# Optimization experiments

Hardware: AMD Instinct MI355X
Metric: run time of the kernel (lower is better)

The kernel has to match this reference:

```python
import jax, jax.numpy as jnp
import numpy as np

N = 512          # input_dim (nodes, fully connected)
T = 16           # time_dim
F = 4            # feature_dim
D = T * F        # node_attr_dim = 64
B = 16           # batch
NEG_SLOPE = 0.2  # GATv2Conv default


def setup_inputs() -> dict:
    key = jax.random.key(0)
    ks = jax.random.split(key, 10)
    s = 0.05
    return {
        "inputs": jax.random.normal(ks[0], (B, N * D), dtype=jnp.float32),
        "Wl": jax.random.normal(ks[1], (D, D), dtype=jnp.float32) * s,  # lin_l weight
        "bl": jax.random.normal(ks[2], (D,), dtype=jnp.float32) * s,
        "Wr": jax.random.normal(ks[3], (D, D), dtype=jnp.float32) * s,  # lin_r weight
        "br": jax.random.normal(ks[4], (D,), dtype=jnp.float32) * s,
        "att": jax.random.normal(ks[5], (D,), dtype=jnp.float32) * s,   # attention vector a
        "bias": jax.random.normal(ks[6], (D,), dtype=jnp.float32) * s,  # GATv2 output bias
        "Wf": jax.random.normal(ks[7], (1, D), dtype=jnp.float32) * s,  # fusion Linear
        "bf": jax.random.normal(ks[8], (1,), dtype=jnp.float32) * s,
    }


def reference(inputs, Wl, bl, Wr, br, att, bias, Wf, bf):
    # GATv2Conv (heads=1) over a fully-connected graph -> dense attention per sample.
    def per_sample(x_flat):
        x = x_flat.reshape(N, D)              # [N, D] node features
        xl = x @ Wl.T + bl                    # source-side transform (lin_l)
        xr = x @ Wr.T + br                    # target-side transform (lin_r)
        # edge (j -> i): e_ij = a . leaky_relu(xl[j] + xr[i])
        s = jax.nn.leaky_relu(xr[:, None, :] + xl[None, :, :], NEG_SLOPE)  # [i, j, d]
        e = jnp.einsum('ijd,d->ij', s, att)   # [N, N] scores
        alpha = jax.nn.softmax(e, axis=-1)    # softmax over sources j per target i
        out = alpha @ xl + bias               # [N, D] aggregated messages
        fused = out @ Wf.T + bf               # [N, 1] fusion linear
        return fused[:, 0]                    # [N]

    return jax.vmap(per_sample)(inputs)       # [B, N]
```

## Files before the change

kernel.cpp:

```cpp
#include <hip/hip_runtime.h>
#include <hip/hip_fp16.h>

#define BB 16
#define NN 512
#define DD 64
#define ROWS (BB * NN)
#define RB 32
#define JCH 32
#define CHUNK (NN / JCH)

static __device__ __forceinline__ __half2 h2bits(unsigned int u) {
    union { unsigned int i; __half2 h; } c; c.i = u; return c.h;
}
static __device__ __forceinline__ unsigned int bits2(__half2 h) {
    union { __half2 h; unsigned int i; } c; c.h = h; return c.i;
}
static __device__ __forceinline__ __half2 absterm(unsigned int s, unsigned int u,
                                                  unsigned int v, __half2 a) {
    return __hfma2(h2bits(s), __habs2(__hadd2(h2bits(u), h2bits(v))), a);
}

__global__ __launch_bounds__(256, 2) void k1_transform(
    const float* __restrict__ x,
    const float* __restrict__ Wl, const float* __restrict__ bl,
    const float* __restrict__ Wr, const float* __restrict__ br,
    const float* __restrict__ att, const float* __restrict__ bias,
    const float* __restrict__ Wf, const float* __restrict__ bf,
    unsigned int* __restrict__ uh, unsigned int* __restrict__ vh,
    float2* __restrict__ epj,
    unsigned int* __restrict__ sgnh, float* __restrict__ cterm)
{
    __shared__ float wt[64][132];
    __shared__ float xst[64][36];
    __shared__ float red[RB][16][2];

    const int tid = threadIdx.x;
    const int r0 = blockIdx.x * RB;

    #pragma unroll
    for (int t = 0; t < 8; ++t) {
        const int idx = t * 256 + tid;
        const int c   = idx & 127;
        const int k4  = (idx >> 7) << 2;
        const float* src = (c < 64) ? (Wl + c * DD + k4) : (Wr + (c - 64) * DD + k4);
        const float4 v = *reinterpret_cast<const float4*>(src);
        wt[k4 + 0][c] = v.x;
        wt[k4 + 1][c] = v.y;
        wt[k4 + 2][c] = v.z;
        wt[k4 + 3][c] = v.w;
    }
    #pragma unroll
    for (int p = 0; p < 2; ++p) {
        const int idx = p * 256 + tid;
        const int row = idx >> 4;
        const int k4  = (idx & 15) << 2;
        const float4 v = *reinterpret_cast<const float4*>(&x[(size_t)(r0 + row) * DD + k4]);
        xst[k4 + 0][row] = v.x;
        xst[k4 + 1][row] = v.y;
        xst[k4 + 2][row] = v.z;
        xst[k4 + 3][row] = v.w;
    }
    __syncthreads();

    const int g  = tid & 31;
    const int rq = tid >> 5;
    const int c0 = g * 4;
    const int ra = rq * 4;
    const bool isL = (c0 < 64);
    const int d0 = c0 & 63;

    const float4 bv = *reinterpret_cast<const float4*>((isL ? bl : br) + d0);
    float acc[4][4];
    #pragma unroll
    for (int r = 0; r < 4; ++r) {
        acc[r][0] = bv.x; acc[r][1] = bv.y; acc[r][2] = bv.z; acc[r][3] = bv.w;
    }

    #pragma unroll 4
    for (int k = 0; k < 64; ++k) {
        const float4 w4 = *reinterpret_cast<const float4*>(&wt[k][c0]);
        const float4 x4 = *reinterpret_cast<const float4*>(&xst[k][ra]);
        acc[0][0] = fmaf(x4.x, w4.x, acc[0][0]);
        acc[0][1] = fmaf(x4.x, w4.y, acc[0][1]);
        acc[0][2] = fmaf(x4.x, w4.z, acc[0][2]);
        acc[0][3] = fmaf(x4.x, w4.w, acc[0][3]);
        acc[1][0] = fmaf(x4.y, w4.x, acc[1][0]);
        acc[1][1] = fmaf(x4.y, w4.y, acc[1][1]);
        acc[1][2] = fmaf(x4.y, w4.z, acc[1][2]);
        acc[1][3] = fmaf(x4.y, w4.w, acc[1][3]);
        acc[2][0] = fmaf(x4.z, w4.x, acc[2][0]);
        acc[2][1] = fmaf(x4.z, w4.y, acc[2][1]);
        acc[2][2] = fmaf(x4.z, w4.z, acc[2][2]);
        acc[2][3] = fmaf(x4.z, w4.w, acc[2][3]);
        acc[3][0] = fmaf(x4.w, w4.x, acc[3][0]);
        acc[3][1] = fmaf(x4.w, w4.y, acc[3][1]);
        acc[3][2] = fmaf(x4.w, w4.z, acc[3][2]);
        acc[3][3] = fmaf(x4.w, w4.w, acc[3][3]);
    }

    const float4 av = *reinterpret_cast<const float4*>(&att[d0]);

    if (isL) {
        const float4 wfv = *reinterpret_cast<const float4*>(&Wf[d0]);
        #pragma unroll
        for (int r = 0; r < 4; ++r) {
            red[ra + r][g][0] = av.x * acc[r][0] + av.y * acc[r][1] + av.z * acc[r][2] + av.w * acc[r][3];
            red[ra + r][g][1] = wfv.x * acc[r][0] + wfv.y * acc[r][1] + wfv.z * acc[r][2] + wfv.w * acc[r][3];
        }
    }

    unsigned int* const dst = isL ? vh : uh;
    const int q    = d0 >> 3;
    const int slot = (d0 & 4) ? 2 : 0;
    const int base = ((r0 >> 9) * 8 + q) * 512 + (r0 & 511);
    #pragma unroll
    for (int r = 0; r < 4; ++r) {
        uint2 pk;
        pk.x = bits2(__floats2half2_rn(0.4f * av.x * acc[r][0], 0.4f * av.y * acc[r][1]));
        pk.y = bits2(__floats2half2_rn(0.4f * av.z * acc[r][2], 0.4f * av.w * acc[r][3]));
        *reinterpret_cast<uint2*>(&dst[(size_t)(base + ra + r) * 4 + slot]) = pk;
    }
    __syncthreads();

    if (tid < RB) {
        float a = 0.f, p = 0.f;
        #pragma unroll
        for (int gg = 0; gg < 16; ++gg) {
            a += red[tid][gg][0];
            p += red[tid][gg][1];
        }
        const float E = __expf(0.6f * a);
        epj[r0 + tid] = make_float2(E, E * p);
    }

    if (blockIdx.x == 0) {
        if (tid < 32) {
            const float s0 = (att[2 * tid]     >= 0.f) ? 1.f : -1.f;
            const float s1 = (att[2 * tid + 1] >= 0.f) ? 1.f : -1.f;
            sgnh[tid] = bits2(__floats2half2_rn(s0, s1));
        }
        if (tid == 0) {
            float ct = bf[0];
            #pragma unroll 8
            for (int d = 0; d < DD; ++d) ct = fmaf(bias[d], Wf[d], ct);
            *cterm = ct;
        }
    }
}

__global__ __launch_bounds__(512, 2) void k2_attn(
    const unsigned int* __restrict__ uh, const unsigned int* __restrict__ vh,
    const float2* __restrict__ epj, const unsigned int* __restrict__ sgnh,
    float2* __restrict__ part)
{
    const int b  = blockIdx.x >> 5;
    const int jc = blockIdx.x & 31;
    const int i  = threadIdx.x;

    uint4 uu[8];
    #pragma unroll
    for (int q = 0; q < 8; ++q)
        uu[q] = *reinterpret_cast<const uint4*>(&uh[(size_t)(((b * 8 + q) << 9) + i) * 4]);

    uint4 sg[8];
    #pragma unroll
    for (int q = 0; q < 8; ++q)
        sg[q] = reinterpret_cast<const uint4*>(sgnh)[q];

    float s = 0.f, sp = 0.f;
    const int j0 = jc * CHUNK;

    #pragma unroll 2
    for (int jj = 0; jj < CHUNK; ++jj) {
        const int j = j0 + jj;
        __half2 a0 = __float2half2_rn(0.f), a1 = a0;
        #pragma unroll
        for (int q = 0; q < 8; ++q) {
            const uint4 vq = *reinterpret_cast<const uint4*>(
                &vh[(size_t)(((b * 8 + q) << 9) + j) * 4]);
            a0 = absterm(sg[q].x, uu[q].x, vq.x, a0);
            a1 = absterm(sg[q].y, uu[q].y, vq.y, a1);
            a0 = absterm(sg[q].z, uu[q].z, vq.z, a0);
            a1 = absterm(sg[q].w, uu[q].w, vq.w, a1);
        }
        const __half2 h = __hadd2(a0, a1);
        const float f = __low2float(h) + __high2float(h);
        const float t = __expf(f);
        const float2 ep = epj[(b << 9) + j];
        s  = fmaf(t, ep.x, s);
        sp = fmaf(t, ep.y, sp);
    }
    part[(size_t)(((b << 5) + jc) << 9) + i] = make_float2(s, sp);
}

__global__ __launch_bounds__(256) void k3_final(
    const float2* __restrict__ part, const float* __restrict__ cterm,
    float* __restrict__ out)
{
    const int t = blockIdx.x * 256 + threadIdx.x;
    const int b = t >> 9, i = t & 511;
    float s = 0.f, sp = 0.f;
    #pragma unroll
    for (int jc = 0; jc < JCH; ++jc) {
        const float2 v = part[(size_t)(((b << 5) + jc) << 9) + i];
        s  += v.x;
        sp += v.y;
    }
    out[t] = sp / s + *cterm;
}

extern "C" void kernel_launch(void* const* d_in, const int* in_sizes, int n_in,
                              void* d_out, int out_size, void* d_ws, size_t ws_size,
                              hipStream_t stream) {
    const float* x    = (const float*)d_in[0];
    const float* Wl   = (const float*)d_in[1];
    const float* bl   = (const float*)d_in[2];
    const float* Wr   = (const float*)d_in[3];
    const float* br   = (const float*)d_in[4];
    const float* att  = (const float*)d_in[5];
    const float* bias = (const float*)d_in[6];
    const float* Wf   = (const float*)d_in[7];
    const float* bf   = (const float*)d_in[8];
    float* out = (float*)d_out;

    unsigned char* ws = (unsigned char*)d_ws;
    unsigned int* uh   = (unsigned int*)ws;
    unsigned int* vh   = uh + (size_t)ROWS * 32;
    float2*       part = (float2*)(vh + (size_t)ROWS * 32);
    float2*       epj  = part + (size_t)BB * JCH * NN;
    unsigned int* sgnh = (unsigned int*)(epj + ROWS);
    float*        ctp  = (float*)(sgnh + 32);

    k1_transform<<<ROWS / RB, 256, 0, stream>>>(x, Wl, bl, Wr, br, att, bias, Wf, bf,
                                                uh, vh, epj, sgnh, ctp);
    k2_attn<<<BB * JCH, 512, 0, stream>>>(uh, vh, epj, sgnh, part);
    k3_final<<<ROWS / 256, 256, 0, stream>>>(part, ctp, out);
}
```

Baseline: 29.72 us.

## Pre-transpose weights in a prep kernel and halve rows per transform block

Result: slower. 34.63 us (+16.5%).

```diff
diff --git a/kernel.cpp b/kernel.cpp
--- a/kernel.cpp
+++ b/kernel.cpp
@@ -5,7 +5,7 @@
 #define NN 512
 #define DD 64
 #define ROWS (BB * NN)
-#define RB 32
+#define RB 16
 #define JCH 32
 #define CHUNK (NN / JCH)
 
@@ -20,40 +20,56 @@
     return __hfma2(h2bits(s), __habs2(__hadd2(h2bits(u), h2bits(v))), a);
 }
 
-__global__ __launch_bounds__(256, 2) void k1_transform(
-    const float* __restrict__ x,
-    const float* __restrict__ Wl, const float* __restrict__ bl,
-    const float* __restrict__ Wr, const float* __restrict__ br,
+__global__ __launch_bounds__(256) void k0_prep(
+    const float* __restrict__ Wl, const float* __restrict__ Wr,
     const float* __restrict__ att, const float* __restrict__ bias,
     const float* __restrict__ Wf, const float* __restrict__ bf,
+    float* __restrict__ wtg, unsigned int* __restrict__ sgnh,
+    float* __restrict__ cterm)
+{
+    const int idx = blockIdx.x * 256 + threadIdx.x;
+    const int c   = idx >> 4;
+    const int k4  = (idx & 15) << 2;
+    const float* src = (c < 64) ? (Wl + c * DD + k4) : (Wr + (c - 64) * DD + k4);
+    const float4 v = *reinterpret_cast<const float4*>(src);
+    wtg[(k4 + 0) * 128 + c] = v.x;
+    wtg[(k4 + 1) * 128 + c] = v.y;
+    wtg[(k4 + 2) * 128 + c] = v.z;
+    wtg[(k4 + 3) * 128 + c] = v.w;
+
+    if (blockIdx.x == 0) {
+        const int tid = threadIdx.x;
+        if (tid < 32) {
+            const float s0 = (att[2 * tid]     >= 0.f) ? 1.f : -1.f;
+            const float s1 = (att[2 * tid + 1] >= 0.f) ? 1.f : -1.f;
+            sgnh[tid] = bits2(__floats2half2_rn(s0, s1));
+        }
+        if (tid == 0) {
+            float ct = bf[0];
+            #pragma unroll 8
+            for (int d = 0; d < DD; ++d) ct = fmaf(bias[d], Wf[d], ct);
+            *cterm = ct;
+        }
+    }
+}
+
+__global__ __launch_bounds__(256) void k1_transform(
+    const float* __restrict__ x, const float* __restrict__ wtg,
+    const float* __restrict__ bl, const float* __restrict__ br,
+    const float* __restrict__ att, const float* __restrict__ Wf,
     unsigned int* __restrict__ uh, unsigned int* __restrict__ vh,
-    float2* __restrict__ epj,
-    unsigned int* __restrict__ sgnh, float* __restrict__ cterm)
-{
-    __shared__ float wt[64][132];
-    __shared__ float xst[64][36];
-    __shared__ float red[RB][16][2];
+    float2* __restrict__ epj)
+{
+    __shared__ float xst[64][20];
+    __shared__ float red[16][16][2];
 
     const int tid = threadIdx.x;
     const int r0 = blockIdx.x * RB;
-
-    #pragma unroll
-    for (int t = 0; t < 8; ++t) {
-        const int idx = t * 256 + tid;
-        const int c   = idx & 127;
-        const int k4  = (idx >> 7) << 2;
-        const float* src = (c < 64) ? (Wl + c * DD + k4) : (Wr + (c - 64) * DD + k4);
-        const float4 v = *reinterpret_cast<const float4*>(src);
-        wt[k4 + 0][c] = v.x;
-        wt[k4 + 1][c] = v.y;
-        wt[k4 + 2][c] = v.z;
-        wt[k4 + 3][c] = v.w;
-    }
-    #pragma unroll
-    for (int p = 0; p < 2; ++p) {
-        const int idx = p * 256 + tid;
-        const int row = idx >> 4;
-        const int k4  = (idx & 15) << 2;
+    const int b  = blockIdx.x >> 5;
+
+    {
+        const int row = tid >> 4;
+        const int k4  = (tid & 15) << 2;
         const float4 v = *reinterpret_cast<const float4*>(&x[(size_t)(r0 + row) * DD + k4]);
         xst[k4 + 0][row] = v.x;
         xst[k4 + 1][row] = v.y;
@@ -65,37 +81,29 @@
     const int g  = tid & 31;
     const int rq = tid >> 5;
     const int c0 = g * 4;
-    const int ra = rq * 4;
+    const int ra = rq * 2;
     const bool isL = (c0 < 64);
     const int d0 = c0 & 63;
 
     const float4 bv = *reinterpret_cast<const float4*>((isL ? bl : br) + d0);
-    float acc[4][4];
-    #pragma unroll
-    for (int r = 0; r < 4; ++r) {
+    float acc[2][4];
+    #pragma unroll
+    for (int r = 0; r < 2; ++r) {
         acc[r][0] = bv.x; acc[r][1] = bv.y; acc[r][2] = bv.z; acc[r][3] = bv.w;
     }
 
     #pragma unroll 4
     for (int k = 0; k < 64; ++k) {
-        const float4 w4 = *reinterpret_cast<const float4*>(&wt[k][c0]);
-        const float4 x4 = *reinterpret_cast<const float4*>(&xst[k][ra]);
-        acc[0][0] = fmaf(x4.x, w4.x, acc[0][0]);
-        acc[0][1] = fmaf(x4.x, w4.y, acc[0][1]);
-        acc[0][2] = fmaf(x4.x, w4.z, acc[0][2]);
-        acc[0][3] = fmaf(x4.x, w4.w, acc[0][3]);
-        acc[1][0] = fmaf(x4.y, w4.x, acc[1][0]);
-        acc[1][1] = fmaf(x4.y, w4.y, acc[1][1]);
-        acc[1][2] = fmaf(x4.y, w4.z, acc[1][2]);
-        acc[1][3] = fmaf(x4.y, w4.w, acc[1][3]);
-        acc[2][0] = fmaf(x4.z, w4.x, acc[2][0]);
-        acc[2][1] = fmaf(x4.z, w4.y, acc[2][1]);
-        acc[2][2] = fmaf(x4.z, w4.z, acc[2][2]);
-        acc[2][3] = fmaf(x4.z, w4.w, acc[2][3]);
-        acc[3][0] = fmaf(x4.w, w4.x, acc[3][0]);
-        acc[3][1] = fmaf(x4.w, w4.y, acc[3][1]);
-        acc[3][2] = fmaf(x4.w, w4.z, acc[3][2]);
-        acc[3][3] = fmaf(x4.w, w4.w, acc[3][3]);
+        const float4 w4 = *reinterpret_cast<const float4*>(&wtg[k * 128 + c0]);
+        const float2 x2 = *reinterpret_cast<const float2*>(&xst[k][ra]);
+        acc[0][0] = fmaf(x2.x, w4.x, acc[0][0]);
+        acc[0][1] = fmaf(x2.x, w4.y, acc[0][1]);
+        acc[0][2] = fmaf(x2.x, w4.z, acc[0][2]);
+        acc[0][3] = fmaf(x2.x, w4.w, acc[0][3]);
+        acc[1][0] = fmaf(x2.y, w4.x, acc[1][0]);
+        acc[1][1] = fmaf(x2.y, w4.y, acc[1][1]);
+        acc[1][2] = fmaf(x2.y, w4.z, acc[1][2]);
+        acc[1][3] = fmaf(x2.y, w4.w, acc[1][3]);
     }
 
     const float4 av = *reinterpret_cast<const float4*>(&att[d0]);
@@ -103,7 +111,7 @@
     if (isL) {
         const float4 wfv = *reinterpret_cast<const float4*>(&Wf[d0]);
         #pragma unroll
-        for (int r = 0; r < 4; ++r) {
+        for (int r = 0; r < 2; ++r) {
             red[ra + r][g][0] = av.x * acc[r][0] + av.y * acc[r][1] + av.z * acc[r][2] + av.w * acc[r][3];
             red[ra + r][g][1] = wfv.x * acc[r][0] + wfv.y * acc[r][1] + wfv.z * acc[r][2] + wfv.w * acc[r][3];
         }
@@ -112,9 +120,9 @@
     unsigned int* const dst = isL ? vh : uh;
     const int q    = d0 >> 3;
     const int slot = (d0 & 4) ? 2 : 0;
-    const int base = ((r0 >> 9) * 8 + q) * 512 + (r0 & 511);
-    #pragma unroll
-    for (int r = 0; r < 4; ++r) {
+    const int base = (b * 8 + q) * 512 + (r0 & 511);
+    #pragma unroll
+    for (int r = 0; r < 2; ++r) {
         uint2 pk;
         pk.x = bits2(__floats2half2_rn(0.4f * av.x * acc[r][0], 0.4f * av.y * acc[r][1]));
         pk.y = bits2(__floats2half2_rn(0.4f * av.z * acc[r][2], 0.4f * av.w * acc[r][3]));
@@ -132,20 +140,6 @@
         const float E = __expf(0.6f * a);
         epj[r0 + tid] = make_float2(E, E * p);
     }
-
-    if (blockIdx.x == 0) {
-        if (tid < 32) {
-            const float s0 = (att[2 * tid]     >= 0.f) ? 1.f : -1.f;
-            const float s1 = (att[2 * tid + 1] >= 0.f) ? 1.f : -1.f;
-            sgnh[tid] = bits2(__floats2half2_rn(s0, s1));
-        }
-        if (tid == 0) {
-            float ct = bf[0];
-            #pragma unroll 8
-            for (int d = 0; d < DD; ++d) ct = fmaf(bias[d], Wf[d], ct);
-            *cterm = ct;
-        }
-    }
 }
 
 __global__ __launch_bounds__(512, 2) void k2_attn(
@@ -170,7 +164,7 @@
     float s = 0.f, sp = 0.f;
     const int j0 = jc * CHUNK;
 
-    #pragma unroll 2
+    #pragma unroll 4
     for (int jj = 0; jj < CHUNK; ++jj) {
         const int j = j0 + jj;
         __half2 a0 = __float2half2_rn(0.f), a1 = a0;
@@ -228,11 +222,12 @@
     unsigned int* vh   = uh + (size_t)ROWS * 32;
     float2*       part = (float2*)(vh + (size_t)ROWS * 32);
     float2*       epj  = part + (size_t)BB * JCH * NN;
-    unsigned int* sgnh = (unsigned int*)(epj + ROWS);
+    float*        wtg  = (float*)(epj + ROWS);
+    unsigned int* sgnh = (unsigned int*)(wtg + 64 * 128);
     float*        ctp  = (float*)(sgnh + 32);
 
-    k1_transform<<<ROWS / RB, 256, 0, stream>>>(x, Wl, bl, Wr, br, att, bias, Wf, bf,
-                                                uh, vh, epj, sgnh, ctp);
+    k0_prep<<<8, 256, 0, stream>>>(Wl, Wr, att, bias, Wf, bf, wtg, sgnh, ctp);
+    k1_transform<<<ROWS / RB, 256, 0, stream>>>(x, wtg, bl, br, att, Wf, uh, vh, epj);
     k2_attn<<<BB * JCH, 512, 0, stream>>>(uh, vh, epj, sgnh, part);
     k3_final<<<ROWS / 256, 256, 0, stream>>>(part, ctp, out);
 }
```
